# Kernel optimization log

Measured on AMD Instinct MI355X. Metric: run time of the kernel, lower is better.

Reference implementation:

```python
import jax, jax.numpy as jnp
import numpy as np

UNITS = 1024
NCLASS = 8000
BATCH = 4096

def setup_inputs() -> dict:
    key = jax.random.key(0)
    k1, k2, k3, k4 = jax.random.split(key, 4)
    inputs = jax.random.randint(k1, (BATCH, 1), 0, NCLASS, dtype=jnp.int32)
    h_tm1 = jax.random.normal(k2, (BATCH, UNITS), dtype=jnp.float32)
    # orthogonal-ish recurrent kernel (scaled normal is fine for a numeric reference)
    recurrent_kernel = jax.random.normal(k3, (UNITS, 4 * UNITS), dtype=jnp.float32) * (1.0 / np.sqrt(UNITS))
    kernel_c = jax.random.normal(k4, (NCLASS, 4 * UNITS), dtype=jnp.float32) * (1.0 / np.sqrt(NCLASS))
    bias_z = jnp.full((UNITS,), 5.0, dtype=jnp.float32)  # initializer=constant(5)
    bias = jnp.zeros((3 * UNITS,), dtype=jnp.float32)
    return {"inputs": inputs, "h_tm1": h_tm1, "recurrent_kernel": recurrent_kernel,
            "kernel_c": kernel_c, "bias_z": bias_z, "bias": bias}

def reference(inputs, h_tm1, recurrent_kernel, kernel_c, bias_z, bias):
    u = h_tm1.shape[-1]
    ch = inputs[:, 0].astype(jnp.int32)
    # one_hot(ch) @ kernel_c == row gather of kernel_c (identical math, O(1) per row)
    c_proj = kernel_c[ch]                      # [B, 4u]
    cz, cr, ch_, co = (c_proj[:, :u], c_proj[:, u:2*u], c_proj[:, 2*u:3*u], c_proj[:, 3*u:])
    Rz, Rr, Rh, Ro = (recurrent_kernel[:, :u], recurrent_kernel[:, u:2*u],
                      recurrent_kernel[:, 2*u:3*u], recurrent_kernel[:, 3*u:])
    z = jax.nn.sigmoid(h_tm1 @ Rz + cz + bias_z)
    r = jax.nn.sigmoid(h_tm1 @ Rr + cr + bias[:u])
    hh = jnp.tanh((r * h_tm1) @ Rh + ch_ + bias[u:2*u])
    h = z * h_tm1 + (1.0 - z) * hh
    o = jnp.tanh(h @ Ro + co + bias[2*u:])
    return (o, h)
```

## Files before the change

### kernel.cpp

```cpp
#include <hip/hip_runtime.h>
#include <stdint.h>

#define UNITS 1024
#define BATCH 4096
#define FOURU 4096

typedef __bf16 bf16x8 __attribute__((ext_vector_type(8)));
typedef float f32x4 __attribute__((ext_vector_type(4)));

__device__ __forceinline__ uint16_t f2bf(float f) {
  uint32_t u = __builtin_bit_cast(uint32_t, f);
  u += 0x7FFFu + ((u >> 16) & 1u);
  return (uint16_t)(u >> 16);
}
__device__ __forceinline__ float bf2f(uint16_t b) {
  uint32_t u = ((uint32_t)b) << 16;
  return __builtin_bit_cast(float, u);
}
__device__ __forceinline__ float fsig(float x) {
  return 1.0f / (1.0f + __expf(-x));
}
__device__ __forceinline__ f32x4 mfma16x16x32(bf16x8 a, bf16x8 b, f32x4 c) {
  return __builtin_amdgcn_mfma_f32_16x16x32_bf16(a, b, c, 0, 0, 0);
}

__device__ __forceinline__ void gll16(uint16_t* lds, const uint16_t* g) {
  __builtin_amdgcn_global_load_lds(
      (const __attribute__((address_space(1))) uint32_t*)g,
      (__attribute__((address_space(3))) uint32_t*)lds, 16, 0, 0);
}

__device__ __forceinline__ int fidx(int row, int l4) {
  return row * 4 + (l4 ^ ((row >> 1) & 3));
}

template <int ROWS>
__device__ __forceinline__ void stage32s(const uint16_t* __restrict__ src,
                                         uint16_t* lds, int tid) {
  const int wb = tid & 192;
#pragma unroll
  for (int p = 0; p < ROWS / 64; ++p) {
    const int gi = p * 256 + tid;
    const int row = gi >> 2;
    const int kg = (gi & 3) ^ ((row >> 1) & 3);
    gll16(lds + (p * 256 + wb) * 8, src + row * UNITS + kg * 8);
  }
}

__global__ __launch_bounds__(256) void prep_kernel(const float* __restrict__ h32,
                                                   uint16_t* __restrict__ hbf,
                                                   const float* __restrict__ R,
                                                   uint16_t* __restrict__ RT) {
  __shared__ float t[32][33];
  const int b = blockIdx.x;
  if (b < 4096) {
    const int i = (b * 256 + threadIdx.x) * 4;
    float4 v = *(const float4*)(h32 + i);
    ushort4 o;
    o.x = f2bf(v.x); o.y = f2bf(v.y); o.z = f2bf(v.z); o.w = f2bf(v.w);
    *(ushort4*)(hbf + i) = o;
  } else {
    const int bb = b - 4096;
    const int n0 = (bb & 127) * 32, k0 = (bb >> 7) * 32;
    const int tx = threadIdx.x & 31, ty = threadIdx.x >> 5;
#pragma unroll
    for (int i = 0; i < 4; ++i)
      t[ty + i * 8][tx] = R[(size_t)(k0 + ty + i * 8) * FOURU + n0 + tx];
    __syncthreads();
#pragma unroll
    for (int i = 0; i < 4; ++i)
      RT[(size_t)(n0 + ty + i * 8) * UNITS + k0 + tx] = f2bf(t[tx][ty + i * 8]);
  }
}

__global__ __launch_bounds__(256, 2) void s1_kernel(
    const uint16_t* __restrict__ hbf, const uint16_t* __restrict__ rt,
    const int* __restrict__ idx, const float* __restrict__ kc,
    const float* __restrict__ bz, const float* __restrict__ bias,
    uint16_t* __restrict__ zb, uint16_t* __restrict__ rhb) {
  __shared__ uint16_t sA[2][128 * 32];
  __shared__ uint16_t sB[2][128 * 32];
  const int tid = threadIdx.x;
  const int lane = tid & 63, wave = tid >> 6;
  const int l15 = lane & 15, l4 = lane >> 4;
  const int fid = blockIdx.y * 16 + blockIdx.x;
  const int nid = (fid & 7) * 64 + (fid >> 3);
  const int row0 = (nid & 31) * 128;
  const int col0 = (nid >> 5) * 128;
  const int rb = (wave >> 1) * 64, cb = (wave & 1) * 64;
  const uint16_t* pa = hbf + (size_t)row0 * UNITS;
  const uint16_t* pb = rt + (size_t)col0 * UNITS;
  f32x4 acc[4][4] = {};

  stage32s<128>(pa, sA[0], tid);
  stage32s<128>(pb, sB[0], tid);
  __syncthreads();

  int cur = 0;
  for (int t = 0; t < 32; ++t) {
    if (t < 31) {
      stage32s<128>(pa + (t + 1) * 32, sA[cur ^ 1], tid);
      stage32s<128>(pb + (t + 1) * 32, sB[cur ^ 1], tid);
    }
    const bf16x8* A8 = (const bf16x8*)sA[cur];
    const bf16x8* B8 = (const bf16x8*)sB[cur];
    bf16x8 af[4], bf[4];
#pragma unroll
    for (int m = 0; m < 4; ++m) af[m] = A8[fidx(rb + m * 16 + l15, l4)];
#pragma unroll
    for (int n = 0; n < 4; ++n) bf[n] = B8[fidx(cb + n * 16 + l15, l4)];
#pragma unroll
    for (int m = 0; m < 4; ++m)
#pragma unroll
      for (int n = 0; n < 4; ++n)
        acc[m][n] = mfma16x16x32(af[m], bf[n], acc[m][n]);
    __syncthreads();
    cur ^= 1;
  }

  const bool is_z = (col0 < UNITS);
#pragma unroll
  for (int m = 0; m < 4; ++m) {
#pragma unroll
    for (int q = 0; q < 4; ++q) {
      const int i = row0 + rb + m * 16 + l4 * 4 + q;
      const int ch = idx[i];
      const float* kcrow = kc + (size_t)ch * FOURU;
#pragma unroll
      for (int n = 0; n < 4; ++n) {
        const int jc = col0 + cb + n * 16 + l15;
        const float a = acc[m][n][q];
        if (is_z) {
          float z = fsig(a + kcrow[jc] + bz[jc]);
          zb[(size_t)i * UNITS + jc] = f2bf(z);
        } else {
          const int j = jc - UNITS;
          const size_t ij = (size_t)i * UNITS + j;
          float r = fsig(a + kcrow[jc] + bias[j]);
          rhb[ij] = f2bf(r * bf2f(hbf[ij]));
        }
      }
    }
  }
}

template <int BN, int EPI>
__global__ __launch_bounds__(256, 4) void gemm_kernel(
    const uint16_t* __restrict__ abf, const uint16_t* __restrict__ bt,
    const int* __restrict__ idx, const float* __restrict__ kc,
    const float* __restrict__ bias, const uint16_t* __restrict__ hbf,
    const uint16_t* __restrict__ zb_in, float* __restrict__ out32,
    uint16_t* __restrict__ outbf) {
  constexpr int NF = BN / 32;
  __shared__ uint16_t sA[2][64 * 32];
  __shared__ uint16_t sB[2][BN * 32];
  const int tid = threadIdx.x;
  const int lane = tid & 63, wave = tid >> 6;
  const int l15 = lane & 15, l4 = lane >> 4;
  const int fid = blockIdx.y * 16 + blockIdx.x;
  const int nid = (fid & 7) * 128 + (fid >> 3);
  const int row0 = (nid & 63) * 64;
  const int col0 = (nid >> 6) * BN;
  const int wr = wave >> 1, wc = wave & 1;
  const uint16_t* pa = abf + (size_t)row0 * UNITS;
  const uint16_t* pb = bt + (size_t)col0 * UNITS;
  f32x4 acc[2][NF] = {};

  stage32s<64>(pa, sA[0], tid);
  stage32s<BN>(pb, sB[0], tid);
  __syncthreads();

  int cur = 0;
  for (int t = 0; t < 32; ++t) {
    if (t < 31) {
      stage32s<64>(pa + (t + 1) * 32, sA[cur ^ 1], tid);
      stage32s<BN>(pb + (t + 1) * 32, sB[cur ^ 1], tid);
    }
    const bf16x8* A8 = (const bf16x8*)sA[cur];
    const bf16x8* B8 = (const bf16x8*)sB[cur];
    bf16x8 af[2], bf[NF];
#pragma unroll
    for (int m = 0; m < 2; ++m) af[m] = A8[fidx(wr * 32 + m * 16 + l15, l4)];
#pragma unroll
    for (int n = 0; n < NF; ++n)
      bf[n] = B8[fidx(wc * (BN / 2) + n * 16 + l15, l4)];
#pragma unroll
    for (int m = 0; m < 2; ++m)
#pragma unroll
      for (int n = 0; n < NF; ++n)
        acc[m][n] = mfma16x16x32(af[m], bf[n], acc[m][n]);
    __syncthreads();
    cur ^= 1;
  }

#pragma unroll
  for (int m = 0; m < 2; ++m) {
#pragma unroll
    for (int q = 0; q < 4; ++q) {
      const int i = row0 + wr * 32 + m * 16 + l4 * 4 + q;
      const int ch = idx[i];
      const float* kcrow = kc + (size_t)ch * FOURU;
#pragma unroll
      for (int n = 0; n < NF; ++n) {
        const int jc = col0 + wc * (BN / 2) + n * 16 + l15;
        const float a = acc[m][n][q];
        const size_t ij = (size_t)i * UNITS + jc;
        if (EPI == 1) {
          float hh = tanhf(a + kcrow[2 * UNITS + jc] + bias[UNITS + jc]);
          float z = bf2f(zb_in[ij]);
          float hv = bf2f(hbf[ij]);
          float hn = z * hv + (1.0f - z) * hh;
          out32[ij] = hn;
          outbf[ij] = f2bf(hn);
        } else {
          out32[ij] = tanhf(a + kcrow[3 * UNITS + jc] + bias[2 * UNITS + jc]);
        }
      }
    }
  }
}

extern "C" void kernel_launch(void* const* d_in, const int* in_sizes, int n_in,
                              void* d_out, int out_size, void* d_ws, size_t ws_size,
                              hipStream_t stream) {
  const int* idx = (const int*)d_in[0];
  const float* h32 = (const float*)d_in[1];
  const float* R = (const float*)d_in[2];
  const float* kc = (const float*)d_in[3];
  const float* bz = (const float*)d_in[4];
  const float* bias = (const float*)d_in[5];

  float* o_out = (float*)d_out;
  float* h_out = o_out + (size_t)BATCH * UNITS;

  uint16_t* hbf = (uint16_t*)d_ws;
  uint16_t* rt = hbf + (size_t)BATCH * UNITS;
  uint16_t* rhb = rt + (size_t)FOURU * UNITS;
  uint16_t* hnb = rhb + (size_t)BATCH * UNITS;
  uint16_t* zbuf = hnb + (size_t)BATCH * UNITS;

  prep_kernel<<<dim3(8192), 256, 0, stream>>>(h32, hbf, R, rt);

  s1_kernel<<<dim3(16, 32), 256, 0, stream>>>(hbf, rt, idx, kc, bz, bias,
                                              zbuf, rhb);

  gemm_kernel<64, 1><<<dim3(16, 64), 256, 0, stream>>>(
      rhb, rt + (size_t)2 * UNITS * UNITS, idx, kc, bias, hbf, zbuf, h_out,
      hnb);

  gemm_kernel<64, 2><<<dim3(16, 64), 256, 0, stream>>>(
      hnb, rt + (size_t)3 * UNITS * UNITS, idx, kc, bias, nullptr, nullptr,
      o_out, nullptr);
}
```

Measured before the change: 119.2 us.

## Overlap Rh/Ro transpose with z/r GEMM, shrink tiles, prefetch gathered bias rows

The prep kernel now transposes only the z/r quarter of the recurrent kernel. The s1 kernel gains extra blocks that transpose the Rh/Ro half, so that work runs alongside the first GEMM. The s1 GEMM tile drops from 128x128 to 64x128 with higher occupancy. The later GEMMs cache gathered indices in LDS and prefetch the kernel_c rows and bias before the K loop, hiding the gather latency behind the MMA work. The tradeoff is smaller tiles with less data reuse and a heterogeneous grid in s1.

After: 103.7 us. 13.0% less time.

```diff
diff --git a/kernel.cpp b/kernel.cpp
--- a/kernel.cpp
+++ b/kernel.cpp
@@ -47,11 +47,25 @@
   }
 }
 
+__device__ __forceinline__ void trans_tile(const float* __restrict__ R,
+                                           uint16_t* __restrict__ RT, int n0,
+                                           int k0, void* smem, int tid) {
+  float(*t)[33] = (float(*)[33])smem;
+  const int tx = tid & 31, ty = tid >> 5;
+#pragma unroll
+  for (int i2 = 0; i2 < 4; ++i2)
+    t[ty + i2 * 8][tx] = R[(size_t)(k0 + ty + i2 * 8) * FOURU + n0 + tx];
+  __syncthreads();
+#pragma unroll
+  for (int i2 = 0; i2 < 4; ++i2)
+    RT[(size_t)(n0 + ty + i2 * 8) * UNITS + k0 + tx] = f2bf(t[tx][ty + i2 * 8]);
+}
+
 __global__ __launch_bounds__(256) void prep_kernel(const float* __restrict__ h32,
                                                    uint16_t* __restrict__ hbf,
                                                    const float* __restrict__ R,
                                                    uint16_t* __restrict__ RT) {
-  __shared__ float t[32][33];
+  __shared__ __align__(16) float t[32][33];
   const int b = blockIdx.x;
   if (b < 4096) {
     const int i = (b * 256 + threadIdx.x) * 4;
@@ -60,75 +74,77 @@
     o.x = f2bf(v.x); o.y = f2bf(v.y); o.z = f2bf(v.z); o.w = f2bf(v.w);
     *(ushort4*)(hbf + i) = o;
   } else {
-    const int bb = b - 4096;
-    const int n0 = (bb & 127) * 32, k0 = (bb >> 7) * 32;
-    const int tx = threadIdx.x & 31, ty = threadIdx.x >> 5;
-#pragma unroll
-    for (int i = 0; i < 4; ++i)
-      t[ty + i * 8][tx] = R[(size_t)(k0 + ty + i * 8) * FOURU + n0 + tx];
-    __syncthreads();
-#pragma unroll
-    for (int i = 0; i < 4; ++i)
-      RT[(size_t)(n0 + ty + i * 8) * UNITS + k0 + tx] = f2bf(t[tx][ty + i * 8]);
-  }
-}
-
-__global__ __launch_bounds__(256, 2) void s1_kernel(
-    const uint16_t* __restrict__ hbf, const uint16_t* __restrict__ rt,
-    const int* __restrict__ idx, const float* __restrict__ kc,
-    const float* __restrict__ bz, const float* __restrict__ bias,
+    const int tt = b - 4096;
+    trans_tile(R, RT, (tt & 63) * 32, (tt >> 6) * 32, t, threadIdx.x);
+  }
+}
+
+__global__ __launch_bounds__(256, 4) void s1_kernel(
+    const uint16_t* __restrict__ hbf, uint16_t* rt, const int* __restrict__ idx,
+    const float* __restrict__ kc, const float* __restrict__ bz,
+    const float* __restrict__ bias, const float* __restrict__ R,
     uint16_t* __restrict__ zb, uint16_t* __restrict__ rhb) {
-  __shared__ uint16_t sA[2][128 * 32];
-  __shared__ uint16_t sB[2][128 * 32];
+  __shared__ __align__(16) char smem[24 * 1024 + 256];
   const int tid = threadIdx.x;
+  const int fid = blockIdx.x;
+
+  if (fid >= 1024) {
+    const int tt = fid - 1024;
+    trans_tile(R, rt, 2048 + (tt & 63) * 32, (tt >> 6) * 32, smem, tid);
+    return;
+  }
+
+  uint16_t* sA = (uint16_t*)smem;
+  uint16_t* sB = (uint16_t*)(smem + 8192);
+  int* sIdx = (int*)(smem + 24 * 1024);
   const int lane = tid & 63, wave = tid >> 6;
   const int l15 = lane & 15, l4 = lane >> 4;
-  const int fid = blockIdx.y * 16 + blockIdx.x;
-  const int nid = (fid & 7) * 64 + (fid >> 3);
-  const int row0 = (nid & 31) * 128;
-  const int col0 = (nid >> 5) * 128;
-  const int rb = (wave >> 1) * 64, cb = (wave & 1) * 64;
+  const int nid = (fid & 7) * 128 + (fid >> 3);
+  const int row0 = (nid & 63) * 64;
+  const int col0 = (nid >> 6) * 128;
+  const int wr = wave >> 1, wc = wave & 1;
   const uint16_t* pa = hbf + (size_t)row0 * UNITS;
   const uint16_t* pb = rt + (size_t)col0 * UNITS;
-  f32x4 acc[4][4] = {};
-
-  stage32s<128>(pa, sA[0], tid);
-  stage32s<128>(pb, sB[0], tid);
+  f32x4 acc[2][4] = {};
+
+  if (tid < 64) sIdx[tid] = idx[row0 + tid];
+  stage32s<64>(pa, sA, tid);
+  stage32s<128>(pb, sB, tid);
   __syncthreads();
 
   int cur = 0;
   for (int t = 0; t < 32; ++t) {
     if (t < 31) {
-      stage32s<128>(pa + (t + 1) * 32, sA[cur ^ 1], tid);
-      stage32s<128>(pb + (t + 1) * 32, sB[cur ^ 1], tid);
-    }
-    const bf16x8* A8 = (const bf16x8*)sA[cur];
-    const bf16x8* B8 = (const bf16x8*)sB[cur];
-    bf16x8 af[4], bf[4];
-#pragma unroll
-    for (int m = 0; m < 4; ++m) af[m] = A8[fidx(rb + m * 16 + l15, l4)];
-#pragma unroll
-    for (int n = 0; n < 4; ++n) bf[n] = B8[fidx(cb + n * 16 + l15, l4)];
-#pragma unroll
-    for (int m = 0; m < 4; ++m)
+      stage32s<64>(pa + (t + 1) * 32, sA + (cur ^ 1) * 2048, tid);
+      stage32s<128>(pb + (t + 1) * 32, sB + (cur ^ 1) * 4096, tid);
+    }
+    const bf16x8* A8 = (const bf16x8*)(sA + cur * 2048);
+    const bf16x8* B8 = (const bf16x8*)(sB + cur * 4096);
+    bf16x8 af[2], bfr[4];
+#pragma unroll
+    for (int m = 0; m < 2; ++m) af[m] = A8[fidx(wr * 32 + m * 16 + l15, l4)];
+#pragma unroll
+    for (int n = 0; n < 4; ++n) bfr[n] = B8[fidx(wc * 64 + n * 16 + l15, l4)];
+#pragma unroll
+    for (int m = 0; m < 2; ++m)
 #pragma unroll
       for (int n = 0; n < 4; ++n)
-        acc[m][n] = mfma16x16x32(af[m], bf[n], acc[m][n]);
+        acc[m][n] = mfma16x16x32(af[m], bfr[n], acc[m][n]);
     __syncthreads();
     cur ^= 1;
   }
 
   const bool is_z = (col0 < UNITS);
 #pragma unroll
-  for (int m = 0; m < 4; ++m) {
+  for (int m = 0; m < 2; ++m) {
 #pragma unroll
     for (int q = 0; q < 4; ++q) {
-      const int i = row0 + rb + m * 16 + l4 * 4 + q;
-      const int ch = idx[i];
-      const float* kcrow = kc + (size_t)ch * FOURU;
+      const int lr = wr * 32 + m * 16 + l4 * 4 + q;
+      const int i = row0 + lr;
+      const float* kcrow = kc + (size_t)sIdx[lr] * FOURU;
 #pragma unroll
       for (int n = 0; n < 4; ++n) {
-        const int jc = col0 + cb + n * 16 + l15;
+        const int jc = col0 + wc * 64 + n * 16 + l15;
         const float a = acc[m][n][q];
         if (is_z) {
           float z = fsig(a + kcrow[jc] + bz[jc]);
@@ -144,51 +160,69 @@
   }
 }
 
-template <int BN, int EPI>
+template <int EPI>
 __global__ __launch_bounds__(256, 4) void gemm_kernel(
     const uint16_t* __restrict__ abf, const uint16_t* __restrict__ bt,
     const int* __restrict__ idx, const float* __restrict__ kc,
     const float* __restrict__ bias, const uint16_t* __restrict__ hbf,
     const uint16_t* __restrict__ zb_in, float* __restrict__ out32,
     uint16_t* __restrict__ outbf) {
-  constexpr int NF = BN / 32;
-  __shared__ uint16_t sA[2][64 * 32];
-  __shared__ uint16_t sB[2][BN * 32];
+  __shared__ __align__(16) char smem[16 * 1024 + 256];
+  uint16_t* sA = (uint16_t*)smem;
+  uint16_t* sB = (uint16_t*)(smem + 8192);
+  int* sIdx = (int*)(smem + 16 * 1024);
   const int tid = threadIdx.x;
   const int lane = tid & 63, wave = tid >> 6;
   const int l15 = lane & 15, l4 = lane >> 4;
-  const int fid = blockIdx.y * 16 + blockIdx.x;
+  const int fid = blockIdx.x;
   const int nid = (fid & 7) * 128 + (fid >> 3);
   const int row0 = (nid & 63) * 64;
-  const int col0 = (nid >> 6) * BN;
+  const int col0 = (nid >> 6) * 64;
   const int wr = wave >> 1, wc = wave & 1;
   const uint16_t* pa = abf + (size_t)row0 * UNITS;
   const uint16_t* pb = bt + (size_t)col0 * UNITS;
-  f32x4 acc[2][NF] = {};
-
-  stage32s<64>(pa, sA[0], tid);
-  stage32s<BN>(pb, sB[0], tid);
+  constexpr int KCOFF = (EPI == 1 ? 2 : 3) * UNITS;
+  constexpr int BOFF = (EPI == 1 ? 1 : 2) * UNITS;
+  f32x4 acc[2][2] = {};
+
+  if (tid < 64) sIdx[tid] = idx[row0 + tid];
+  stage32s<64>(pa, sA, tid);
+  stage32s<64>(pb, sB, tid);
   __syncthreads();
+
+  float kcp[2][4][2], bp[2];
+#pragma unroll
+  for (int n = 0; n < 2; ++n)
+    bp[n] = bias[BOFF + col0 + wc * 32 + n * 16 + l15];
+#pragma unroll
+  for (int m = 0; m < 2; ++m)
+#pragma unroll
+    for (int q = 0; q < 4; ++q) {
+      const int lr = wr * 32 + m * 16 + l4 * 4 + q;
+      const float* kcrow = kc + (size_t)sIdx[lr] * FOURU + KCOFF;
+#pragma unroll
+      for (int n = 0; n < 2; ++n)
+        kcp[m][q][n] = kcrow[col0 + wc * 32 + n * 16 + l15];
+    }
 
   int cur = 0;
   for (int t = 0; t < 32; ++t) {
     if (t < 31) {
-      stage32s<64>(pa + (t + 1) * 32, sA[cur ^ 1], tid);
-      stage32s<BN>(pb + (t + 1) * 32, sB[cur ^ 1], tid);
-    }
-    const bf16x8* A8 = (const bf16x8*)sA[cur];
-    const bf16x8* B8 = (const bf16x8*)sB[cur];
-    bf16x8 af[2], bf[NF];
+      stage32s<64>(pa + (t + 1) * 32, sA + (cur ^ 1) * 2048, tid);
+      stage32s<64>(pb + (t + 1) * 32, sB + (cur ^ 1) * 2048, tid);
+    }
+    const bf16x8* A8 = (const bf16x8*)(sA + cur * 2048);
+    const bf16x8* B8 = (const bf16x8*)(sB + cur * 2048);
+    bf16x8 af[2], bfr[2];
 #pragma unroll
     for (int m = 0; m < 2; ++m) af[m] = A8[fidx(wr * 32 + m * 16 + l15, l4)];
 #pragma unroll
-    for (int n = 0; n < NF; ++n)
-      bf[n] = B8[fidx(wc * (BN / 2) + n * 16 + l15, l4)];
+    for (int n = 0; n < 2; ++n) bfr[n] = B8[fidx(wc * 32 + n * 16 + l15, l4)];
 #pragma unroll
     for (int m = 0; m < 2; ++m)
 #pragma unroll
-      for (int n = 0; n < NF; ++n)
-        acc[m][n] = mfma16x16x32(af[m], bf[n], acc[m][n]);
+      for (int n = 0; n < 2; ++n)
+        acc[m][n] = mfma16x16x32(af[m], bfr[n], acc[m][n]);
     __syncthreads();
     cur ^= 1;
   }
@@ -198,22 +232,20 @@
 #pragma unroll
     for (int q = 0; q < 4; ++q) {
       const int i = row0 + wr * 32 + m * 16 + l4 * 4 + q;
-      const int ch = idx[i];
-      const float* kcrow = kc + (size_t)ch * FOURU;
-#pragma unroll
-      for (int n = 0; n < NF; ++n) {
-        const int jc = col0 + wc * (BN / 2) + n * 16 + l15;
-        const float a = acc[m][n][q];
+#pragma unroll
+      for (int n = 0; n < 2; ++n) {
+        const int jc = col0 + wc * 32 + n * 16 + l15;
         const size_t ij = (size_t)i * UNITS + jc;
+        const float a = acc[m][n][q] + kcp[m][q][n] + bp[n];
         if (EPI == 1) {
-          float hh = tanhf(a + kcrow[2 * UNITS + jc] + bias[UNITS + jc]);
+          float hh = tanhf(a);
           float z = bf2f(zb_in[ij]);
           float hv = bf2f(hbf[ij]);
           float hn = z * hv + (1.0f - z) * hh;
           out32[ij] = hn;
           outbf[ij] = f2bf(hn);
         } else {
-          out32[ij] = tanhf(a + kcrow[3 * UNITS + jc] + bias[2 * UNITS + jc]);
+          out32[ij] = tanhf(a);
         }
       }
     }
@@ -239,16 +271,16 @@
   uint16_t* hnb = rhb + (size_t)BATCH * UNITS;
   uint16_t* zbuf = hnb + (size_t)BATCH * UNITS;
 
-  prep_kernel<<<dim3(8192), 256, 0, stream>>>(h32, hbf, R, rt);
-
-  s1_kernel<<<dim3(16, 32), 256, 0, stream>>>(hbf, rt, idx, kc, bz, bias,
-                                              zbuf, rhb);
-
-  gemm_kernel<64, 1><<<dim3(16, 64), 256, 0, stream>>>(
+  prep_kernel<<<dim3(6144), 256, 0, stream>>>(h32, hbf, R, rt);
+
+  s1_kernel<<<dim3(3072), 256, 0, stream>>>(hbf, rt, idx, kc, bz, bias, R,
+                                            zbuf, rhb);
+
+  gemm_kernel<1><<<dim3(1024), 256, 0, stream>>>(
       rhb, rt + (size_t)2 * UNITS * UNITS, idx, kc, bias, hbf, zbuf, h_out,
       hnb);
 
-  gemm_kernel<64, 2><<<dim3(16, 64), 256, 0, stream>>>(
+  gemm_kernel<2><<<dim3(1024), 256, 0, stream>>>(
       hnb, rt + (size_t)3 * UNITS * UNITS, idx, kc, bias, nullptr, nullptr,
       o_out, nullptr);
 }
```
